# Performance work log

Hardware: AMD Instinct MI355X
Metric: run time of the kernel (lower is better)

## Reference

```python
import jax, jax.numpy as jnp
import numpy as np

B, L, S, D = 32, 256, 4, 512
H = L * S  # history_capacity
TGB = 128
VOCAB = 50000
LN_EPS = 1e-5


def _layer_norm(x, gamma, beta):
    mu = jnp.mean(x, axis=-1, keepdims=True)
    var = jnp.var(x, axis=-1, keepdims=True)
    return (x - mu) * jax.lax.rsqrt(var + LN_EPS) * gamma + beta


def setup_inputs() -> dict:
    key = jax.random.key(0)
    ks = jax.random.split(key, 16)
    inp = {
        'embed_table': jax.random.normal(ks[0], (VOCAB, D), jnp.float32) * 0.02,
        'time_gap_emb': jax.random.normal(ks[1], (TGB + 1, D), jnp.float32) * 0.02,
        'seq_id_emb': jax.random.normal(ks[2], (S + 1, D), jnp.float32) * 0.02,
        'pos_emb': jax.random.normal(ks[3], (L, D), jnp.float32) * 0.02,
        'ln_gamma': jnp.ones((5 * D,), jnp.float32),
        'ln_beta': jnp.zeros((5 * D,), jnp.float32),
        'w1': jax.random.normal(ks[4], (5 * D, 4 * D), jnp.float32) * (1.0 / np.sqrt(5 * D)),
        'b1': jnp.zeros((4 * D,), jnp.float32),
        'w2': jax.random.normal(ks[5], (4 * D, D), jnp.float32) * (1.0 / np.sqrt(4 * D)),
        'b2': jnp.zeros((D,), jnp.float32),
        'empty_tokens': jax.random.normal(ks[6], (S, D), jnp.float32) * 0.02,
        'history_tokens': jax.random.randint(ks[7], (B, H), 0, VOCAB, jnp.int64 if jax.config.jax_enable_x64 else jnp.int32),
        'post_tokens': jax.random.randint(ks[8], (B, H), 0, VOCAB),
        'author_tokens': jax.random.randint(ks[9], (B, H), 0, VOCAB),
        'action_tokens': jax.random.randint(ks[10], (B, H), 0, VOCAB),
        'time_gap': jax.random.randint(ks[11], (B, H), 0, TGB + 1),
        'group_ids': jax.random.randint(ks[12], (B, H), 0, S + 1),
        'lengths': jax.random.randint(ks[13], (B,), 0, H + 1),
    }
    return inp


def reference(embed_table, time_gap_emb, seq_id_emb, pos_emb, ln_gamma, ln_beta,
              w1, b1, w2, b2, empty_tokens,
              history_tokens, post_tokens, author_tokens, action_tokens,
              time_gap, group_ids, lengths):
    # padded-dense validity mask: positions < lengths  [B,H]
    history_mask = jnp.arange(H)[None, :] < lengths[:, None]
    # zero out padded tokens (to_padded_dense pads with 0)
    hm_i = history_mask.astype(history_tokens.dtype)
    ht = history_tokens * hm_i
    pt = post_tokens * hm_i
    at = author_tokens * hm_i
    ct = action_tokens * hm_i
    tg = jnp.clip(time_gap * hm_i, 0, TGB)
    gid = group_ids * hm_i

    # event feature: 4 token embeds + time-gap embed -> [B,H,5D]
    event_inputs = jnp.concatenate(
        [embed_table[ht], embed_table[pt], embed_table[at], embed_table[ct],
         time_gap_emb[tg]], axis=-1)
    x = _layer_norm(event_inputs, ln_gamma, ln_beta)
    h = jax.nn.silu(x @ w1 + b1)          # dropout is eval-mode no-op
    event_tokens = h @ w2 + b2            # [B,H,D]

    # per-(batch, group) bucketization: keep last L valid positions of each group
    grp = jnp.arange(1, S + 1)
    mask_bs = history_mask[:, None, :] & (gid[:, None, :] == grp[None, :, None])  # [B,S,H]
    cum = jnp.cumsum(mask_bs.astype(jnp.int32), axis=-1)
    count = cum[..., -1]                                  # [B,S]
    offset = jnp.maximum(count - L, 0)                    # drop all but last L
    rank0 = cum - 1
    keep = mask_bs & (rank0 >= offset[..., None])
    dest = jnp.where(keep, rank0 - offset[..., None], L)  # slot L = dump slot

    def scatter_one(tokens, d):  # tokens [H,D], d [H] -> [L,D]
        return jnp.zeros((L + 1, D), tokens.dtype).at[d].set(tokens)[:L]

    # vmap over batch then group
    states = jax.vmap(lambda tok, ds: jax.vmap(lambda d: scatter_one(tok, d))(ds))(
        event_tokens, dest)                               # [B,S,L,D]

    # empty groups get the learned empty token at slot 0
    is_empty = (count == 0)                               # [B,S]
    slot0 = (jnp.arange(L) == 0)                          # [L]
    states = jnp.where((is_empty[:, :, None] & slot0[None, None, :])[..., None],
                       empty_tokens[None, :, None, :], states)
    kept = jnp.where(is_empty, 1, jnp.minimum(count, L))  # [B,S]
    sequence_mask = jnp.arange(L)[None, None, :] < kept[..., None]  # [B,S,L]

    states = states + pos_emb[None, None, :, :] + seq_id_emb[1:][None, :, None, :]
    states = states * sequence_mask[..., None].astype(states.dtype)
    return states, sequence_mask
```

## Files before the change

kernel.cpp:

```cpp
#include <hip/hip_runtime.h>
#include <hip/hip_bf16.h>
#include <stdint.h>

#define NB 32
#define NL 256
#define NS 4
#define ND 512
#define NH 1024
#define FIVE_D 2560
#define HID 2048
#define MMAX 32768

typedef __bf16 bf16_t;
typedef __bf16 bf16x4 __attribute__((ext_vector_type(4)));
typedef __bf16 bf16x8 __attribute__((ext_vector_type(8)));
typedef float f32x4 __attribute__((ext_vector_type(4)));

__device__ __forceinline__ void async_ld16(const void* g, void* l) {
  __builtin_amdgcn_global_load_lds(
      (__attribute__((address_space(1))) void*)(uintptr_t)g,
      (__attribute__((address_space(3))) void*)(uintptr_t)l, 16, 0, 0);
}

__global__ void build_index_kernel(const int* __restrict__ group_ids,
                                   const int* __restrict__ lengths,
                                   int* __restrict__ n_rows,
                                   int* __restrict__ row_src,
                                   int* __restrict__ row_dst,
                                   const float* __restrict__ empty_tokens,
                                   const float* __restrict__ pos_emb,
                                   const float* __restrict__ seq_emb,
                                   float* __restrict__ out,
                                   float* __restrict__ mask) {
  const int g = blockIdx.x >> 2;
  const int qtr = blockIdx.x & 3;
  const int b = g >> 2, s = g & 3;
  const int t = threadIdx.x;
  const int lane = t & 63, w = t >> 6;
  int len = lengths[b];
  len = len < 0 ? 0 : (len > NH ? NH : len);
  const int* gi = group_ids + b * NH;

  __shared__ int wtot[16];
  __shared__ int sbase;

  bool valid[4];
#pragma unroll
  for (int c = 0; c < 4; ++c) {
    int h = c * 256 + t;
    valid[c] = (h < len) && (gi[h] == s + 1);
    unsigned long long m = __ballot(valid[c]);
    if (lane == 0) wtot[c * 4 + w] = __popcll(m);
  }
  __syncthreads();

  int pre[16];
  int run = 0;
#pragma unroll
  for (int i = 0; i < 16; ++i) { pre[i] = run; run += wtot[i]; }
  const int count = run;
  const int keff = count < NL ? count : NL;
  const int offset = count - keff;

  const bool empty = (count == 0);
  const int start = empty ? 1 : keff;

  if (qtr == 0) {
    if (t == 0) sbase = atomicAdd(n_rows, keff);
    __syncthreads();
    const int base = sbase;

    const unsigned long long lt = (1ull << lane) - 1ull;
#pragma unroll
    for (int c = 0; c < 4; ++c) {
      unsigned long long m = __ballot(valid[c]);
      if (valid[c]) {
        int rank = pre[c * 4 + w] + __popcll(m & lt);
        if (rank >= offset) {
          int slot = rank - offset;
          row_src[base + slot] = b * NH + c * 256 + t;
          row_dst[base + slot] = g * NL + slot;
        }
      }
    }

    const int keptm = empty ? 1 : keff;
    mask[g * NL + t] = (t < keptm) ? 1.f : 0.f;

    if (empty) {
      float* basep = out + (size_t)g * NL * ND;
      for (int d = t; d < ND; d += 256)
        basep[d] = empty_tokens[s * ND + d] + pos_emb[d] +
                   seq_emb[(s + 1) * ND + d];
    }
  }

  int lo = qtr * 64; if (lo < start) lo = start;
  const int hi = qtr * 64 + 64;
  if (lo < hi) {
    uint4* p = (uint4*)(out + (size_t)g * NL * ND);
    uint4 z; z.x = z.y = z.z = z.w = 0u;
    for (int i = lo * (ND / 4) + t; i < hi * (ND / 4); i += 256) p[i] = z;
  }
}

template <int KD, int NDIM>
__global__ void transpose_cvt_kernel(const float* __restrict__ src,
                                     bf16_t* __restrict__ dst) {
  __shared__ float tile[32][33];
  int k0 = blockIdx.y * 32, n0 = blockIdx.x * 32;
  int tx = threadIdx.x & 31, ty = threadIdx.x >> 5;
#pragma unroll
  for (int i = 0; i < 32; i += 8)
    tile[ty + i][tx] = src[(size_t)(k0 + ty + i) * NDIM + n0 + tx];
  __syncthreads();
#pragma unroll
  for (int i = 0; i < 32; i += 8)
    dst[(size_t)(n0 + ty + i) * KD + k0 + tx] = (bf16_t)tile[tx][ty + i];
}

__launch_bounds__(256)
__global__ void gather_ln_kernel(const float* __restrict__ embed,
                                 const float* __restrict__ tg_emb,
                                 const int* __restrict__ ht,
                                 const int* __restrict__ pt,
                                 const int* __restrict__ at,
                                 const int* __restrict__ ct,
                                 const int* __restrict__ tg,
                                 const float* __restrict__ gamma,
                                 const float* __restrict__ beta,
                                 const int* __restrict__ n_rows,
                                 const int* __restrict__ row_src,
                                 int row_base, int chunk,
                                 bf16_t* __restrict__ X) {
  const int l = threadIdx.x & 63;
  const int wid = blockIdx.x * 4 + (threadIdx.x >> 6);
  const int wstride = gridDim.x * 4;
  const int M = *n_rows;
  int lim = row_base + chunk;
  if (lim > M) lim = M;

  const int o = l * 4;

  for (int r = row_base + wid; r < lim; r += wstride) {
    const int rl = r - row_base;
    const int pos = row_src[r];

    const float* s0 = embed + (size_t)ht[pos] * ND;
    const float* s1 = embed + (size_t)pt[pos] * ND;
    const float* s2 = embed + (size_t)at[pos] * ND;
    const float* s3 = embed + (size_t)ct[pos] * ND;
    int tgv = tg[pos];
    tgv = tgv < 0 ? 0 : (tgv > 128 ? 128 : tgv);
    const float* s4 = tg_emb + (size_t)tgv * ND;

    float4 v0 = *(const float4*)(s0 + o);
    float4 v1 = *(const float4*)(s0 + 256 + o);
    float4 v2 = *(const float4*)(s1 + o);
    float4 v3 = *(const float4*)(s1 + 256 + o);
    float4 v4 = *(const float4*)(s2 + o);
    float4 v5 = *(const float4*)(s2 + 256 + o);
    float4 v6 = *(const float4*)(s3 + o);
    float4 v7 = *(const float4*)(s3 + 256 + o);
    float4 v8 = *(const float4*)(s4 + o);
    float4 v9 = *(const float4*)(s4 + 256 + o);

    float sum = 0.f, sq = 0.f;
#define ACC(vk)                                                              \
    do {                                                                     \
      sum += vk.x + vk.y + vk.z + vk.w;                                      \
      sq += vk.x * vk.x + vk.y * vk.y + vk.z * vk.z + vk.w * vk.w;           \
    } while (0)
    ACC(v0); ACC(v1); ACC(v2); ACC(v3); ACC(v4);
    ACC(v5); ACC(v6); ACC(v7); ACC(v8); ACC(v9);
#undef ACC
#pragma unroll
    for (int off = 32; off > 0; off >>= 1) {
      sum += __shfl_xor(sum, off);
      sq += __shfl_xor(sq, off);
    }
    const float mu = sum * (1.f / FIVE_D);
    const float var = sq * (1.f / FIVE_D) - mu * mu;
    const float rstd = rsqrtf(var + 1e-5f);

    bf16_t* xr = X + (size_t)rl * FIVE_D;
#define LN_STORE(vk, kofs)                                                   \
    do {                                                                     \
      float4 gm = *(const float4*)(gamma + (kofs) + o);                      \
      float4 bt = *(const float4*)(beta + (kofs) + o);                       \
      bf16x4 ov;                                                             \
      ov[0] = (bf16_t)((vk.x - mu) * rstd * gm.x + bt.x);                    \
      ov[1] = (bf16_t)((vk.y - mu) * rstd * gm.y + bt.y);                    \
      ov[2] = (bf16_t)((vk.z - mu) * rstd * gm.z + bt.z);                    \
      ov[3] = (bf16_t)((vk.w - mu) * rstd * gm.w + bt.w);                    \
      *(bf16x4*)(xr + (kofs) + o) = ov;                                      \
    } while (0)
    LN_STORE(v0, 0);    LN_STORE(v1, 256);
    LN_STORE(v2, 512);  LN_STORE(v3, 768);
    LN_STORE(v4, 1024); LN_STORE(v5, 1280);
    LN_STORE(v6, 1536); LN_STORE(v7, 1792);
    LN_STORE(v8, 2048); LN_STORE(v9, 2304);
#undef LN_STORE
  }
}

#define FENCE asm volatile("" ::: "memory")
#define BARRIER do { FENCE; __builtin_amdgcn_s_barrier(); FENCE; } while (0)
#define WAIT_VM(n) asm volatile("s_waitcnt vmcnt(" #n ")" ::: "memory")

template <int KD, int LDC>
__launch_bounds__(512, 2)
__global__ void gemm256_kernel(const bf16_t* __restrict__ A,
                               const bf16_t* __restrict__ Bt,
                               const int* __restrict__ nrows_p,
                               int row_base,
                               const float* __restrict__ bias,
                               bf16_t* __restrict__ Cb) {
  static_assert(KD % 64 == 0 && KD / 64 >= 2, "KD");
  const int M = *nrows_p;
  const int m0 = blockIdx.x * 256;
  if (row_base + m0 >= M) return;
  const int n0 = blockIdx.y * 256;

  extern __shared__ char smem[];

  const int t = threadIdx.x;
  const int lane = t & 63;
  const int wv = t >> 6;
  const int wm = wv >> 2;
  const int wn = wv & 3;
  const int l15 = lane & 15;
  const int l4 = lane >> 4;

  const int r0 = t >> 3;
  const int sq = (t & 7) ^ (r0 & 7);
  const bf16_t* Ab = A + (size_t)(m0 + r0) * KD + sq * 8;
  const bf16_t* Bb = Bt + (size_t)(n0 + r0) * KD + sq * 8;
  const int dst16 = t * 16;

  const int cs0 = (l4 ^ (l15 & 7)) << 4;
  const int cs1 = cs0 ^ 64;
  const int arow = (wm * 128 + l15) * 128;
  const int brow = (wn * 64 + l15) * 128;

  f32x4 acc[2][2][4][2] = {};
  bf16x8 a[4][2], bl[2][2], bh[2][2];

#define STAGE_A(dbuf, h, kofs)                                               \
  do {                                                                       \
    char* _d = smem + (dbuf) * 65536 + (h) * 16384 + dst16;                  \
    async_ld16(Ab + (size_t)((h) * 128) * KD + (kofs), _d);                  \
    async_ld16(Ab + (size_t)((h) * 128 + 64) * KD + (kofs), _d + 8192);      \
  } while (0)
#define STAGE_B(dbuf, h, kofs)                                               \
  do {                                                                       \
    char* _d = smem + (dbuf) * 65536 + 32768 + (h) * 16384 + dst16;          \
    async_ld16(Bb + (size_t)((h) * 128) * KD + (kofs), _d);                  \
    async_ld16(Bb + (size_t)((h) * 128 + 64) * KD + (kofs), _d + 8192);      \
  } while (0)
#define LOAD_A(cbuf, mh)                                                     \
  do {                                                                       \
    const char* _s = smem + (cbuf) * 65536 + (mh) * 8192 + arow;             \
    _Pragma("unroll") for (int _i = 0; _i < 4; ++_i) {                       \
      a[_i][0] = *(const bf16x8*)(_s + _i * 2048 + cs0);                     \
      a[_i][1] = *(const bf16x8*)(_s + _i * 2048 + cs1);                     \
    }                                                                        \
  } while (0)
#define LOAD_B(dst, cbuf, nh)                                                \
  do {                                                                       \
    const char* _s = smem + (cbuf) * 65536 + 32768 + (nh) * 4096 + brow;     \
    _Pragma("unroll") for (int _j = 0; _j < 2; ++_j) {                       \
      dst[_j][0] = *(const bf16x8*)(_s + _j * 2048 + cs0);                   \
      dst[_j][1] = *(const bf16x8*)(_s + _j * 2048 + cs1);                   \
    }                                                                        \
  } while (0)
#define MMA(mh, nh, B)                                                       \
  do {                                                                       \
    _Pragma("unroll") for (int _i = 0; _i < 4; ++_i)                         \
    _Pragma("unroll") for (int _j = 0; _j < 2; ++_j) {                       \
      acc[mh][nh][_i][_j] = __builtin_amdgcn_mfma_f32_16x16x32_bf16(         \
          a[_i][0], B[_j][0], acc[mh][nh][_i][_j], 0, 0, 0);                 \
      acc[mh][nh][_i][_j] = __builtin_amdgcn_mfma_f32_16x16x32_bf16(         \
          a[_i][1], B[_j][1], acc[mh][nh][_i][_j], 0, 0, 0);                 \
    }                                                                        \
  } while (0)

  constexpr int NT = KD / 64;

  STAGE_A(0, 0, 0);
  STAGE_A(0, 1, 0);
  STAGE_B(0, 0, 0);
  STAGE_B(0, 1, 0);

  int c = 0;
  for (int tk = 1; tk < NT; ++tk) {
    const int kn = tk * 64;
    const int d = c ^ 1;
    STAGE_A(d, 0, kn);
    STAGE_A(d, 1, kn);
    WAIT_VM(4);
    BARRIER;
    LOAD_A(c, 0);
    LOAD_B(bl, c, 0);
    __builtin_amdgcn_s_setprio(1);
    MMA(0, 0, bl);
    __builtin_amdgcn_s_setprio(0);
    STAGE_B(d, 0, kn);
    STAGE_B(d, 1, kn);
    LOAD_B(bh, c, 1);
    __builtin_amdgcn_s_setprio(1);
    MMA(0, 1, bh);
    __builtin_amdgcn_s_setprio(0);
    LOAD_A(c, 1);
    __builtin_amdgcn_s_setprio(1);
    MMA(1, 1, bh);
    MMA(1, 0, bl);
    __builtin_amdgcn_s_setprio(0);
    BARRIER;
    c = d;
  }

  WAIT_VM(0);
  BARRIER;
  LOAD_A(c, 0);
  LOAD_B(bl, c, 0);
  MMA(0, 0, bl);
  LOAD_B(bh, c, 1);
  MMA(0, 1, bh);
  LOAD_A(c, 1);
  MMA(1, 1, bh);
  MMA(1, 0, bl);

#pragma unroll
  for (int mh = 0; mh < 2; ++mh)
#pragma unroll
    for (int i = 0; i < 4; ++i) {
      const int rbase = m0 + wm * 128 + mh * 64 + i * 16 + l4 * 4;
#pragma unroll
      for (int nh = 0; nh < 2; ++nh)
#pragma unroll
        for (int j = 0; j < 2; ++j) {
          const int n = n0 + wn * 64 + nh * 32 + j * 16 + l15;
          const float bn = bias[n];
#pragma unroll
          for (int q = 0; q < 4; ++q) {
            float v = acc[mh][nh][i][j][q] + bn;
            v = v / (1.f + __expf(-v));
            Cb[(size_t)(rbase + q) * LDC + n] = (bf16_t)v;
          }
        }
    }
#undef STAGE_A
#undef STAGE_B
#undef LOAD_A
#undef LOAD_B
#undef MMA
}

template <int KD>
__launch_bounds__(512, 2)
__global__ void gemm128_scatter_kernel(const bf16_t* __restrict__ A,
                                       const bf16_t* __restrict__ Bt,
                                       const int* __restrict__ nrows_p,
                                       int row_base,
                                       const float* __restrict__ bias,
                                       const int* __restrict__ row_dst,
                                       const float* __restrict__ pos_emb,
                                       const float* __restrict__ seq_emb,
                                       float* __restrict__ out) {
  static_assert(KD % 64 == 0 && KD / 64 >= 2, "KD");
  const int M = *nrows_p;
  const int m0 = blockIdx.x * 128;
  if (row_base + m0 >= M) return;
  const int n0 = blockIdx.y * 128;

  extern __shared__ char smem[];

  const int t = threadIdx.x;
  const int lane = t & 63;
  const int wv = t >> 6;
  const int wm = wv >> 1;
  const int wn = wv & 1;
  const int l15 = lane & 15;
  const int l4 = lane >> 4;

  const int r0 = t >> 3;
  const int sq = (t & 7) ^ (r0 & 7);
  const bf16_t* Ab = A + (size_t)(m0 + r0) * KD + sq * 8;
  const bf16_t* Bb = Bt + (size_t)(n0 + r0) * KD + sq * 8;
  const int dst16 = t * 16;

  const int cs0 = (l4 ^ (l15 & 7)) << 4;
  const int cs1 = cs0 ^ 64;
  const int arow = (wm * 32 + l15) * 128;
  const int brow = (wn * 64 + l15) * 128;

  f32x4 acc[2][4] = {};
  bf16x8 a[2][2], b[4][2];

#define STAGE_A2(dbuf, kofs)                                                 \
  do {                                                                       \
    char* _d = smem + (dbuf) * 32768 + dst16;                                \
    async_ld16(Ab + (kofs), _d);                                             \
    async_ld16(Ab + (size_t)64 * KD + (kofs), _d + 8192);                    \
  } while (0)
#define STAGE_B2(dbuf, kofs)                                                 \
  do {                                                                       \
    char* _d = smem + (dbuf) * 32768 + 16384 + dst16;                        \
    async_ld16(Bb + (kofs), _d);                                             \
    async_ld16(Bb + (size_t)64 * KD + (kofs), _d + 8192);                    \
  } while (0)
#define LOAD_A2(cbuf)                                                        \
  do {                                                                       \
    const char* _s = smem + (cbuf) * 32768 + arow;                           \
    _Pragma("unroll") for (int _i = 0; _i < 2; ++_i) {                       \
      a[_i][0] = *(const bf16x8*)(_s + _i * 2048 + cs0);                     \
      a[_i][1] = *(const bf16x8*)(_s + _i * 2048 + cs1);                     \
    }                                                                        \
  } while (0)
#define LOAD_B2(cbuf)                                                        \
  do {                                                                       \
    const char* _s = smem + (cbuf) * 32768 + 16384 + brow;                   \
    _Pragma("unroll") for (int _j = 0; _j < 4; ++_j) {                       \
      b[_j][0] = *(const bf16x8*)(_s + _j * 2048 + cs0);                     \
      b[_j][1] = *(const bf16x8*)(_s + _j * 2048 + cs1);                     \
    }                                                                        \
  } while (0)
#define MMA2                                                                 \
  do {                                                                       \
    _Pragma("unroll") for (int _i = 0; _i < 2; ++_i)                         \
    _Pragma("unroll") for (int _j = 0; _j < 4; ++_j) {                       \
      acc[_i][_j] = __builtin_amdgcn_mfma_f32_16x16x32_bf16(                 \
          a[_i][0], b[_j][0], acc[_i][_j], 0, 0, 0);                         \
      acc[_i][_j] = __builtin_amdgcn_mfma_f32_16x16x32_bf16(                 \
          a[_i][1], b[_j][1], acc[_i][_j], 0, 0, 0);                         \
    }                                                                        \
  } while (0)

  constexpr int NT = KD / 64;

  STAGE_A2(0, 0);
  STAGE_B2(0, 0);

  int c = 0;
  for (int tk = 1; tk < NT; ++tk) {
    const int kn = tk * 64;
    const int d = c ^ 1;
    STAGE_A2(d, kn);
    WAIT_VM(2);
    BARRIER;
    LOAD_A2(c);
    LOAD_B2(c);
    STAGE_B2(d, kn);
    __builtin_amdgcn_s_setprio(1);
    MMA2;
    __builtin_amdgcn_s_setprio(0);
    BARRIER;
    c = d;
  }

  WAIT_VM(0);
  BARRIER;
  LOAD_A2(c);
  LOAD_B2(c);
  MMA2;

#pragma unroll
  for (int i = 0; i < 2; ++i) {
    int mbase = m0 + wm * 32 + i * 16 + l4 * 4;
#pragma unroll
    for (int q = 0; q < 4; ++q) {
      int r = mbase + q;
      if (row_base + r >= M) continue;
      int dst = row_dst[row_base + r];
      int slot = dst & (NL - 1);
      int sg = (dst >> 8) & 3;
#pragma unroll
      for (int j = 0; j < 4; ++j) {
        int n = n0 + wn * 64 + j * 16 + l15;
        float v = acc[i][j][q] + bias[n] + pos_emb[slot * ND + n] +
                  seq_emb[(sg + 1) * ND + n];
        out[(size_t)dst * ND + n] = v;
      }
    }
  }
#undef STAGE_A2
#undef STAGE_B2
#undef LOAD_A2
#undef LOAD_B2
#undef MMA2
}

extern "C" void kernel_launch(void* const* d_in, const int* in_sizes, int n_in,
                              void* d_out, int out_size, void* d_ws,
                              size_t ws_size, hipStream_t stream) {
  const float* embed_table = (const float*)d_in[0];
  const float* time_gap_emb = (const float*)d_in[1];
  const float* seq_id_emb = (const float*)d_in[2];
  const float* pos_emb = (const float*)d_in[3];
  const float* ln_gamma = (const float*)d_in[4];
  const float* ln_beta = (const float*)d_in[5];
  const float* w1 = (const float*)d_in[6];
  const float* b1 = (const float*)d_in[7];
  const float* w2 = (const float*)d_in[8];
  const float* b2 = (const float*)d_in[9];
  const float* empty_tokens = (const float*)d_in[10];
  const int* history_tokens = (const int*)d_in[11];
  const int* post_tokens = (const int*)d_in[12];
  const int* author_tokens = (const int*)d_in[13];
  const int* action_tokens = (const int*)d_in[14];
  const int* time_gap = (const int*)d_in[15];
  const int* group_ids = (const int*)d_in[16];
  const int* lengths = (const int*)d_in[17];

  const size_t fixed = 266240 + (size_t)(HID * FIVE_D + ND * HID) * 2;
  int chunk, nchunk;
  if (ws_size >= fixed + (size_t)32768 * 9216) { chunk = 32768; nchunk = 1; }
  else if (ws_size >= fixed + (size_t)16384 * 9216) { chunk = 16384; nchunk = 2; }
  else { chunk = 8192; nchunk = 4; }

  char* ws = (char*)d_ws;
  int* n_rows = (int*)ws;
  int* row_src = (int*)(ws + 4096);
  int* row_dst = (int*)(ws + 4096 + 131072);
  bf16_t* W1T = (bf16_t*)(ws + 266240);
  bf16_t* W2T = W1T + (size_t)HID * FIVE_D;
  bf16_t* Xc = W2T + (size_t)ND * HID;
  bf16_t* H1c = Xc + (size_t)chunk * FIVE_D;

  float* out_states = (float*)d_out;
  float* out_mask = out_states + (size_t)NB * NS * NL * ND;

  (void)hipFuncSetAttribute(
      reinterpret_cast<const void*>(gemm256_kernel<FIVE_D, HID>),
      hipFuncAttributeMaxDynamicSharedMemorySize, 131072);
  (void)hipFuncSetAttribute(
      reinterpret_cast<const void*>(gemm128_scatter_kernel<HID>),
      hipFuncAttributeMaxDynamicSharedMemorySize, 65536);

  hipMemsetAsync(n_rows, 0, 4, stream);

  build_index_kernel<<<NB * NS * 4, 256, 0, stream>>>(
      group_ids, lengths, n_rows, row_src, row_dst, empty_tokens, pos_emb,
      seq_id_emb, out_states, out_mask);

  transpose_cvt_kernel<FIVE_D, HID>
      <<<dim3(HID / 32, FIVE_D / 32), 256, 0, stream>>>(w1, W1T);
  transpose_cvt_kernel<HID, ND>
      <<<dim3(ND / 32, HID / 32), 256, 0, stream>>>(w2, W2T);

  for (int c = 0; c < nchunk; ++c) {
    int row_base = c * chunk;
    gather_ln_kernel<<<2048, 256, 0, stream>>>(
        embed_table, time_gap_emb, history_tokens, post_tokens, author_tokens,
        action_tokens, time_gap, ln_gamma, ln_beta, n_rows, row_src, row_base,
        chunk, Xc);

    gemm256_kernel<FIVE_D, HID>
        <<<dim3(chunk / 256, HID / 256), 512, 131072, stream>>>(
            Xc, W1T, n_rows, row_base, b1, H1c);

    gemm128_scatter_kernel<HID>
        <<<dim3(chunk / 128, ND / 128), 512, 65536, stream>>>(
            H1c, W2T, n_rows, row_base, b2, row_dst, pos_emb, seq_id_emb,
            out_states);
  }
}
```

Before: 395.8 us.

## Split GEMM1 K-loop prefetch into four phased stages with interleaved barriers

Reorganizes the first GEMM's shared-memory tiling so each quarter of the A and B tiles is staged separately. Global-to-LDS loads for the next K step are issued between MFMA phases, each guarded by its own waitcnt and barrier, instead of all at once. This is meant to spread memory traffic across the compute and overlap it more evenly. It adds extra barriers per iteration, and the second GEMM's launch bound is raised to 4 waves per SIMD, which may limit registers.

```diff
diff --git a/kernel.cpp b/kernel.cpp
--- a/kernel.cpp
+++ b/kernel.cpp
@@ -210,12 +210,12 @@
 
 template <int KD, int LDC>
 __launch_bounds__(512, 2)
-__global__ void gemm256_kernel(const bf16_t* __restrict__ A,
-                               const bf16_t* __restrict__ Bt,
-                               const int* __restrict__ nrows_p,
-                               int row_base,
-                               const float* __restrict__ bias,
-                               bf16_t* __restrict__ Cb) {
+__global__ void gemm256p4_kernel(const bf16_t* __restrict__ A,
+                                 const bf16_t* __restrict__ Bt,
+                                 const int* __restrict__ nrows_p,
+                                 int row_base,
+                                 const float* __restrict__ bias,
+                                 bf16_t* __restrict__ Cb) {
   static_assert(KD % 64 == 0 && KD / 64 >= 2, "KD");
   const int M = *nrows_p;
   const int m0 = blockIdx.x * 256;
@@ -235,130 +235,141 @@
   const int r0 = t >> 3;
   const int sq = (t & 7) ^ (r0 & 7);
   const bf16_t* Ab = A + (size_t)(m0 + r0) * KD + sq * 8;
-  const bf16_t* Bb = Bt + (size_t)(n0 + r0) * KD + sq * 8;
+  const bf16_t* Bb =
+      Bt + (size_t)(n0 + (r0 >> 5) * 64 + (r0 & 31)) * KD + sq * 8;
   const int dst16 = t * 16;
 
   const int cs0 = (l4 ^ (l15 & 7)) << 4;
   const int cs1 = cs0 ^ 64;
-  const int arow = (wm * 128 + l15) * 128;
-  const int brow = (wn * 64 + l15) * 128;
+  const int arow = (wm * 64 + l15) * 128;
+  const int brow = (wn * 32 + l15) * 128;
 
   f32x4 acc[2][2][4][2] = {};
   bf16x8 a[4][2], bl[2][2], bh[2][2];
 
-#define STAGE_A(dbuf, h, kofs)                                               \
+#define SA(dbuf, h, kofs)                                                    \
   do {                                                                       \
     char* _d = smem + (dbuf) * 65536 + (h) * 16384 + dst16;                  \
-    async_ld16(Ab + (size_t)((h) * 128) * KD + (kofs), _d);                  \
-    async_ld16(Ab + (size_t)((h) * 128 + 64) * KD + (kofs), _d + 8192);      \
-  } while (0)
-#define STAGE_B(dbuf, h, kofs)                                               \
+    async_ld16(Ab + (size_t)((h) * 64) * KD + (kofs), _d);                   \
+    async_ld16(Ab + (size_t)((h) * 64 + 128) * KD + (kofs), _d + 8192);      \
+  } while (0)
+#define SB(dbuf, h, kofs)                                                    \
   do {                                                                       \
     char* _d = smem + (dbuf) * 65536 + 32768 + (h) * 16384 + dst16;          \
-    async_ld16(Bb + (size_t)((h) * 128) * KD + (kofs), _d);                  \
-    async_ld16(Bb + (size_t)((h) * 128 + 64) * KD + (kofs), _d + 8192);      \
-  } while (0)
-#define LOAD_A(cbuf, mh)                                                     \
-  do {                                                                       \
-    const char* _s = smem + (cbuf) * 65536 + (mh) * 8192 + arow;             \
+    async_ld16(Bb + (size_t)((h) * 32) * KD + (kofs), _d);                   \
+    async_ld16(Bb + (size_t)((h) * 32 + 128) * KD + (kofs), _d + 8192);      \
+  } while (0)
+#define LA(cbuf, ih)                                                         \
+  do {                                                                       \
+    const char* _s = smem + (cbuf) * 65536 + (ih) * 16384 + arow;            \
     _Pragma("unroll") for (int _i = 0; _i < 4; ++_i) {                       \
       a[_i][0] = *(const bf16x8*)(_s + _i * 2048 + cs0);                     \
       a[_i][1] = *(const bf16x8*)(_s + _i * 2048 + cs1);                     \
     }                                                                        \
   } while (0)
-#define LOAD_B(dst, cbuf, nh)                                                \
-  do {                                                                       \
-    const char* _s = smem + (cbuf) * 65536 + 32768 + (nh) * 4096 + brow;     \
+#define LB(dst, cbuf, jh)                                                    \
+  do {                                                                       \
+    const char* _s = smem + (cbuf) * 65536 + 32768 + (jh) * 16384 + brow;    \
     _Pragma("unroll") for (int _j = 0; _j < 2; ++_j) {                       \
       dst[_j][0] = *(const bf16x8*)(_s + _j * 2048 + cs0);                   \
       dst[_j][1] = *(const bf16x8*)(_s + _j * 2048 + cs1);                   \
     }                                                                        \
   } while (0)
-#define MMA(mh, nh, B)                                                       \
+#define MMA(ih, jh, B)                                                       \
   do {                                                                       \
     _Pragma("unroll") for (int _i = 0; _i < 4; ++_i)                         \
     _Pragma("unroll") for (int _j = 0; _j < 2; ++_j) {                       \
-      acc[mh][nh][_i][_j] = __builtin_amdgcn_mfma_f32_16x16x32_bf16(         \
-          a[_i][0], B[_j][0], acc[mh][nh][_i][_j], 0, 0, 0);                 \
-      acc[mh][nh][_i][_j] = __builtin_amdgcn_mfma_f32_16x16x32_bf16(         \
-          a[_i][1], B[_j][1], acc[mh][nh][_i][_j], 0, 0, 0);                 \
+      acc[ih][jh][_i][_j] = __builtin_amdgcn_mfma_f32_16x16x32_bf16(         \
+          a[_i][0], B[_j][0], acc[ih][jh][_i][_j], 0, 0, 0);                 \
+      acc[ih][jh][_i][_j] = __builtin_amdgcn_mfma_f32_16x16x32_bf16(         \
+          a[_i][1], B[_j][1], acc[ih][jh][_i][_j], 0, 0, 0);                 \
     }                                                                        \
   } while (0)
 
   constexpr int NT = KD / 64;
 
-  STAGE_A(0, 0, 0);
-  STAGE_A(0, 1, 0);
-  STAGE_B(0, 0, 0);
-  STAGE_B(0, 1, 0);
+  SA(0, 0, 0);
+  SB(0, 0, 0);
+  SB(0, 1, 0);
+  SA(0, 1, 0);
 
   int c = 0;
   for (int tk = 1; tk < NT; ++tk) {
     const int kn = tk * 64;
     const int d = c ^ 1;
-    STAGE_A(d, 0, kn);
-    STAGE_A(d, 1, kn);
     WAIT_VM(4);
     BARRIER;
-    LOAD_A(c, 0);
-    LOAD_B(bl, c, 0);
+    LA(c, 0);
+    LB(bl, c, 0);
+    SA(d, 0, kn);
     __builtin_amdgcn_s_setprio(1);
     MMA(0, 0, bl);
     __builtin_amdgcn_s_setprio(0);
-    STAGE_B(d, 0, kn);
-    STAGE_B(d, 1, kn);
-    LOAD_B(bh, c, 1);
+    WAIT_VM(4);
+    BARRIER;
+    LB(bh, c, 1);
+    SB(d, 0, kn);
     __builtin_amdgcn_s_setprio(1);
     MMA(0, 1, bh);
     __builtin_amdgcn_s_setprio(0);
-    LOAD_A(c, 1);
+    WAIT_VM(4);
+    BARRIER;
+    LA(c, 1);
+    SB(d, 1, kn);
     __builtin_amdgcn_s_setprio(1);
     MMA(1, 1, bh);
+    __builtin_amdgcn_s_setprio(0);
+    SA(d, 1, kn);
+    __builtin_amdgcn_s_setprio(1);
     MMA(1, 0, bl);
     __builtin_amdgcn_s_setprio(0);
     BARRIER;
     c = d;
   }
 
+  WAIT_VM(4);
+  BARRIER;
+  LA(c, 0);
+  LB(bl, c, 0);
+  MMA(0, 0, bl);
+  WAIT_VM(2);
+  BARRIER;
+  LB(bh, c, 1);
+  MMA(0, 1, bh);
   WAIT_VM(0);
   BARRIER;
-  LOAD_A(c, 0);
-  LOAD_B(bl, c, 0);
-  MMA(0, 0, bl);
-  LOAD_B(bh, c, 1);
-  MMA(0, 1, bh);
-  LOAD_A(c, 1);
+  LA(c, 1);
   MMA(1, 1, bh);
   MMA(1, 0, bl);
 
 #pragma unroll
-  for (int mh = 0; mh < 2; ++mh)
+  for (int ih = 0; ih < 2; ++ih)
 #pragma unroll
     for (int i = 0; i < 4; ++i) {
-      const int rbase = m0 + wm * 128 + mh * 64 + i * 16 + l4 * 4;
-#pragma unroll
-      for (int nh = 0; nh < 2; ++nh)
+      const int rbase = m0 + wm * 128 + ih * 64 + i * 16 + l4 * 4;
+#pragma unroll
+      for (int jh = 0; jh < 2; ++jh)
 #pragma unroll
         for (int j = 0; j < 2; ++j) {
-          const int n = n0 + wn * 64 + nh * 32 + j * 16 + l15;
+          const int n = n0 + wn * 64 + jh * 32 + j * 16 + l15;
           const float bn = bias[n];
 #pragma unroll
           for (int q = 0; q < 4; ++q) {
-            float v = acc[mh][nh][i][j][q] + bn;
+            float v = acc[ih][jh][i][j][q] + bn;
             v = v / (1.f + __expf(-v));
             Cb[(size_t)(rbase + q) * LDC + n] = (bf16_t)v;
           }
         }
     }
-#undef STAGE_A
-#undef STAGE_B
-#undef LOAD_A
-#undef LOAD_B
+#undef SA
+#undef SB
+#undef LA
+#undef LB
 #undef MMA
 }
 
 template <int KD>
-__launch_bounds__(512, 2)
+__launch_bounds__(512, 4)
 __global__ void gemm128_scatter_kernel(const bf16_t* __restrict__ A,
                                        const bf16_t* __restrict__ Bt,
                                        const int* __restrict__ nrows_p,
@@ -532,7 +543,7 @@
   float* out_mask = out_states + (size_t)NB * NS * NL * ND;
 
   (void)hipFuncSetAttribute(
-      reinterpret_cast<const void*>(gemm256_kernel<FIVE_D, HID>),
+      reinterpret_cast<const void*>(gemm256p4_kernel<FIVE_D, HID>),
       hipFuncAttributeMaxDynamicSharedMemorySize, 131072);
   (void)hipFuncSetAttribute(
       reinterpret_cast<const void*>(gemm128_scatter_kernel<HID>),
@@ -556,7 +567,7 @@
         action_tokens, time_gap, ln_gamma, ln_beta, n_rows, row_src, row_base,
         chunk, Xc);
 
-    gemm256_kernel<FIVE_D, HID>
+    gemm256p4_kernel<FIVE_D, HID>
         <<<dim3(chunk / 256, HID / 256), 512, 131072, stream>>>(
             Xc, W1T, n_rows, row_base, b1, H1c);
 
```

Measured after the change: 392.6 us (median of 2 runs). No clear change (-0.8%).
